# Kernel tuning notes

Measured on AMD Instinct MI355X. Metric: run time of the kernel, lower is better.

Reference implementation:

```python
import jax, jax.numpy as jnp
import numpy as np

B, S, D, H = 8, 1024, 512, 8
DK = D // H
NEG = -1e30  # stands in for -inf; masked probs are zero-filled afterwards, so math matches


def setup_inputs() -> dict:
    rng = jax.random.key(0)
    ks = jax.random.split(rng, 12)
    f = lambda k, shape: jax.random.normal(k, shape, dtype=jnp.float32)
    w = lambda k: f(k, (D, D)) * 0.02  # stored as (in, out); y = x @ W + b
    return {
        "query": f(ks[0], (B, S, D)),
        "key": f(ks[1], (B, S, D)),
        "value": f(ks[2], (B, S, D)),
        "mask": jax.random.randint(ks[3], (B, 1, S), 0, 2, dtype=jnp.int32),
        "Wq": w(ks[4]), "bq": jnp.zeros((D,), jnp.float32),
        "Wk": w(ks[5]), "bk": jnp.zeros((D,), jnp.float32),
        "Wv": w(ks[6]), "bv": jnp.zeros((D,), jnp.float32),
        "Wo": w(ks[7]), "bo": jnp.zeros((D,), jnp.float32),
    }


def reference(query, key, value, mask, Wq, bq, Wk, bk, Wv, bv, Wo, bo):
    # QKV projections -> (B, H, S, DK)
    def proj(x, W, b):
        return (x @ W + b).reshape(B, -1, H, DK).transpose(0, 2, 1, 3)

    q = proj(query, Wq, bq)
    k = proj(key, Wk, bk)
    v = proj(value, Wv, bv)

    scores = jnp.einsum("bhqd,bhkd->bhqk", q, k) / jnp.sqrt(jnp.float32(DK))
    m = (mask[:, None, :, :] == 0)  # (B, 1, 1, S): True where masked out
    scores = jnp.where(m, NEG, scores)
    attn = jax.nn.softmax(scores, axis=-1)
    attn = jnp.where(m, 0.0, attn)  # dropout rate is 0.0 -> identity

    x = jnp.einsum("bhqk,bhkd->bhqd", attn, v)
    x = x.transpose(0, 2, 1, 3).reshape(B, -1, D)  # (B, S, D)
    return x @ Wo + bo
```

## Files before the change

kernel.cpp:

```cpp
#include <hip/hip_runtime.h>
#include <hip/hip_bf16.h>

#define NB 8
#define NS 1024
#define ND 512
#define NH 8
#define NDK 64

typedef __attribute__((ext_vector_type(8))) short bf16x8;
typedef __attribute__((ext_vector_type(4))) short s16x4;
typedef __attribute__((ext_vector_type(4))) float f32x4;
typedef __attribute__((ext_vector_type(16))) float f32x16;

#define QSCALE 0.18033688011112042f
#define NEGBIG -3.0e38f

#define CVTPK(dst, a, b) \
    asm("v_cvt_pk_bf16_f32 %0, %1, %2" : "=v"(dst) : "v"(a), "v"(b))
#define PLSWAP(a, b) \
    asm("v_permlane32_swap_b32 %0, %1" : "+v"(a), "+v"(b))

__device__ __forceinline__ unsigned short bfround(float f) {
    union { float f; unsigned u; } v; v.f = f;
    unsigned u = v.u;
    u += 0x7fffu + ((u >> 16) & 1u);
    return (unsigned short)(u >> 16);
}

__device__ __forceinline__ size_t qf_off(int s, int dk) {
    return ((size_t)(((s >> 5) * 4 + (dk >> 4)) * 64 + ((dk >> 3) & 1) * 32 + (s & 31)) << 3) + (dk & 7);
}
__device__ __forceinline__ size_t kf_off(int s, int dk) {
    return ((size_t)(((s >> 6) * 8 + ((s >> 5) & 1) * 4 + (dk >> 4)) * 64 + ((dk >> 3) & 1) * 32 + (s & 31)) << 3) + (dk & 7);
}
__device__ __forceinline__ size_t vf_off(int s, int dk) {
    return ((size_t)(((s >> 6) * 8 + (dk >> 5) * 4 + ((s >> 4) & 3)) * 64 + ((s >> 3) & 1) * 32 + (dk & 31)) << 3) + (s & 7);
}

__global__ __launch_bounds__(256) void wt_kernel(const float* __restrict__ W0,
                                                 const float* __restrict__ W1,
                                                 const float* __restrict__ W2,
                                                 const float* __restrict__ W3,
                                                 unsigned short* __restrict__ wt) {
    __shared__ float sh[64][65];
    const int z = blockIdx.z;
    const float* W = z == 0 ? W0 : z == 1 ? W1 : z == 2 ? W2 : W3;
    unsigned short* out = wt + (size_t)z * ND * ND;
    const int o0 = blockIdx.x * 64, i0 = blockIdx.y * 64;
    const int tx = threadIdx.x & 63;
    const int ty = threadIdx.x >> 6;
    #pragma unroll
    for (int rr = 0; rr < 16; ++rr) {
        const int row = ty * 16 + rr;
        sh[row][tx] = W[(size_t)(i0 + row) * ND + o0 + tx];
    }
    __syncthreads();
    #pragma unroll
    for (int rr = 0; rr < 16; ++rr) {
        const int row = ty * 16 + rr;
        out[(size_t)(o0 + row) * ND + i0 + tx] = bfround(sh[tx][row]);
    }
}

template <bool A_F32, bool OUT_F32>
__global__ __launch_bounds__(256) void gemm_kernel(
    const void* __restrict__ A0, const void* __restrict__ A1, const void* __restrict__ A2,
    const unsigned short* __restrict__ wt_base, int wt_stride,
    const float* __restrict__ b0, const float* __restrict__ b1, const float* __restrict__ b2,
    void* __restrict__ out_base, size_t out_stride_bytes) {
    __shared__ unsigned short As[128][40];
    __shared__ unsigned short Bs[128][40];
    const int t = threadIdx.x;
    const int lane = t & 63, w = t >> 6;
    const int wr = w >> 1, wc = w & 1;
    const int lr = lane & 15, lg = lane >> 4;
    const int bid = blockIdx.x;
    const int u = (bid & 7) * (gridDim.x >> 3) + (bid >> 3);
    const int xt = u & 3, yt = (u >> 2) & 63, z = u >> 8;
    const void* Ap = z == 0 ? A0 : z == 1 ? A1 : A2;
    const float* bias = z == 0 ? b0 : z == 1 ? b1 : b2;
    const unsigned short* Wt = wt_base + (size_t)z * wt_stride;
    void* outp = (void*)((char*)out_base + (size_t)z * out_stride_bytes);
    const int m0 = yt * 128, n0 = xt * 128;

    f32x4 acc[4][4];
    #pragma unroll
    for (int i = 0; i < 4; ++i)
        #pragma unroll
        for (int j = 0; j < 4; ++j) acc[i][j] = (f32x4){0.f, 0.f, 0.f, 0.f};

    for (int kt = 0; kt < 16; ++kt) {
        const int k0 = kt * 32;
        __syncthreads();
        if (A_F32) {
            const float* A = (const float*)Ap;
            const int mrow = t >> 3, k4 = (t & 7) * 4;
            #pragma unroll
            for (int r = 0; r < 4; ++r) {
                const int m = mrow + 32 * r;
                float4 v = *(const float4*)(A + (size_t)(m0 + m) * ND + k0 + k4);
                unsigned p0, p1;
                CVTPK(p0, v.x, v.y);
                CVTPK(p1, v.z, v.w);
                uint2 pv; pv.x = p0; pv.y = p1;
                *(uint2*)(&As[m][k4]) = pv;
            }
        } else {
            const unsigned short* A = (const unsigned short*)Ap;
            #pragma unroll
            for (int r = 0; r < 2; ++r) {
                const int idx = t + 256 * r;
                const int m = idx >> 2, k8 = (idx & 3) * 8;
                *(bf16x8*)(&As[m][k8]) =
                    *(const bf16x8*)(A + (size_t)(m0 + m) * ND + k0 + k8);
            }
        }
        #pragma unroll
        for (int r = 0; r < 2; ++r) {
            const int idx = t + 256 * r;
            const int n = idx >> 2, k8 = (idx & 3) * 8;
            *(bf16x8*)(&Bs[n][k8]) =
                *(const bf16x8*)(Wt + (size_t)(n0 + n) * ND + k0 + k8);
        }
        __syncthreads();
        bf16x8 af[4], bfv[4];
        #pragma unroll
        for (int mi = 0; mi < 4; ++mi)
            af[mi] = *(const bf16x8*)(&As[wr * 64 + mi * 16 + lr][lg * 8]);
        #pragma unroll
        for (int nj = 0; nj < 4; ++nj)
            bfv[nj] = *(const bf16x8*)(&Bs[wc * 64 + nj * 16 + lr][lg * 8]);
        #pragma unroll
        for (int mi = 0; mi < 4; ++mi)
            #pragma unroll
            for (int nj = 0; nj < 4; ++nj)
                acc[mi][nj] = __builtin_amdgcn_mfma_f32_16x16x32_bf16(
                    af[mi], bfv[nj], acc[mi][nj], 0, 0, 0);
    }

    const float osc = (!OUT_F32 && z == 0) ? QSCALE : 1.0f;
    #pragma unroll
    for (int mi = 0; mi < 4; ++mi) {
        #pragma unroll
        for (int nj = 0; nj < 4; ++nj) {
            const int n = n0 + wc * 64 + nj * 16 + lr;
            const float bv = bias[n];
            #pragma unroll
            for (int r = 0; r < 4; ++r) {
                const int m = m0 + wr * 64 + mi * 16 + lg * 4 + r;
                const float val = (acc[mi][nj][r] + bv) * osc;
                if (OUT_F32) {
                    ((float*)outp)[(size_t)m * ND + n] = val;
                } else {
                    const int bb = m >> 10, s = m & 1023;
                    const int hh = n >> 6, dk = n & 63;
                    const size_t off = z == 0 ? qf_off(s, dk)
                                     : z == 1 ? kf_off(s, dk)
                                              : vf_off(s, dk);
                    ((unsigned short*)outp)[((size_t)(bb * NH + hh) << 16) + off] =
                        bfround(val);
                }
            }
        }
    }
}

struct AttnState {
    f32x16 acc0, acc1;
    float m_st, l_st;
};

__device__ __forceinline__ void attn_step(const bf16x8 (&kf)[8], const bf16x8 (&vv)[8],
                                          const bf16x8 (&qf)[4], int mval,
                                          float* __restrict__ brow, int lane, int hi,
                                          AttnState& st) {
    brow[lane] = mval ? 0.f : NEGBIG;

    f32x16 sc0 = {}, sc1 = {};
    __builtin_amdgcn_s_setprio(1);
    sc0 = __builtin_amdgcn_mfma_f32_32x32x16_bf16(kf[0], qf[0], sc0, 0, 0, 0);
    sc1 = __builtin_amdgcn_mfma_f32_32x32x16_bf16(kf[4], qf[0], sc1, 0, 0, 0);
    sc0 = __builtin_amdgcn_mfma_f32_32x32x16_bf16(kf[1], qf[1], sc0, 0, 0, 0);
    sc1 = __builtin_amdgcn_mfma_f32_32x32x16_bf16(kf[5], qf[1], sc1, 0, 0, 0);
    sc0 = __builtin_amdgcn_mfma_f32_32x32x16_bf16(kf[2], qf[2], sc0, 0, 0, 0);
    sc1 = __builtin_amdgcn_mfma_f32_32x32x16_bf16(kf[6], qf[2], sc1, 0, 0, 0);
    sc0 = __builtin_amdgcn_mfma_f32_32x32x16_bf16(kf[3], qf[3], sc0, 0, 0, 0);
    sc1 = __builtin_amdgcn_mfma_f32_32x32x16_bf16(kf[7], qf[3], sc1, 0, 0, 0);
    __builtin_amdgcn_s_setprio(0);

    {
        const float* bl = brow + 4 * hi;
        #pragma unroll
        for (int mm = 0; mm < 4; ++mm) {
            const f32x4 bv0 = *(const f32x4*)(bl + 8 * mm);
            const f32x4 bv1 = *(const f32x4*)(bl + 32 + 8 * mm);
            #pragma unroll
            for (int c = 0; c < 4; ++c) {
                sc0[4 * mm + c] += bv0[c];
                sc1[4 * mm + c] += bv1[c];
            }
        }
    }

    float tv[16];
    #pragma unroll
    for (int r = 0; r < 16; ++r) tv[r] = fmaxf(sc0[r], sc1[r]);
    #pragma unroll
    for (int s = 8; s > 0; s >>= 1)
        #pragma unroll
        for (int r = 0; r < 16; ++r)
            if (r < s) tv[r] = fmaxf(tv[r], tv[r + s]);
    const float mx = fmaxf(tv[0], __shfl_xor(tv[0], 32));
    const float mn = fmaxf(st.m_st, mx);

    #pragma unroll
    for (int r = 0; r < 16; ++r) {
        sc0[r] = __builtin_amdgcn_exp2f(sc0[r] - mn);
        sc1[r] = __builtin_amdgcn_exp2f(sc1[r] - mn);
    }
    #pragma unroll
    for (int r = 0; r < 16; ++r) tv[r] = sc0[r] + sc1[r];
    #pragma unroll
    for (int s = 8; s > 0; s >>= 1)
        #pragma unroll
        for (int r = 0; r < 16; ++r)
            if (r < s) tv[r] += tv[r + s];
    const float rs = tv[0] + __shfl_xor(tv[0], 32);

    const bool ch = mn > st.m_st;
    if (__any(ch)) {
        const float f = __builtin_amdgcn_exp2f(st.m_st - mn);
        st.l_st = st.l_st * f + rs;
        st.m_st = mn;
        #pragma unroll
        for (int r = 0; r < 16; ++r) { st.acc0[r] *= f; st.acc1[r] *= f; }
    } else {
        st.l_st += rs;
    }

    union U8 { unsigned u[4]; bf16x8 v; };
    bf16x8 pA0, pA1, pB0, pB1;
    {
        unsigned w00, w01, w10, w11, w20, w21, w30, w31;
        CVTPK(w00, sc0[0], sc0[1]);  CVTPK(w01, sc0[2], sc0[3]);
        CVTPK(w10, sc0[4], sc0[5]);  CVTPK(w11, sc0[6], sc0[7]);
        CVTPK(w20, sc0[8], sc0[9]);  CVTPK(w21, sc0[10], sc0[11]);
        CVTPK(w30, sc0[12], sc0[13]); CVTPK(w31, sc0[14], sc0[15]);
        PLSWAP(w00, w10); PLSWAP(w01, w11);
        PLSWAP(w20, w30); PLSWAP(w21, w31);
        U8 f0; f0.u[0] = w00; f0.u[1] = w01; f0.u[2] = w10; f0.u[3] = w11;
        U8 f1; f1.u[0] = w20; f1.u[1] = w21; f1.u[2] = w30; f1.u[3] = w31;
        pA0 = f0.v; pA1 = f1.v;
    }
    {
        unsigned w00, w01, w10, w11, w20, w21, w30, w31;
        CVTPK(w00, sc1[0], sc1[1]);  CVTPK(w01, sc1[2], sc1[3]);
        CVTPK(w10, sc1[4], sc1[5]);  CVTPK(w11, sc1[6], sc1[7]);
        CVTPK(w20, sc1[8], sc1[9]);  CVTPK(w21, sc1[10], sc1[11]);
        CVTPK(w30, sc1[12], sc1[13]); CVTPK(w31, sc1[14], sc1[15]);
        PLSWAP(w00, w10); PLSWAP(w01, w11);
        PLSWAP(w20, w30); PLSWAP(w21, w31);
        U8 f0; f0.u[0] = w00; f0.u[1] = w01; f0.u[2] = w10; f0.u[3] = w11;
        U8 f1; f1.u[0] = w20; f1.u[1] = w21; f1.u[2] = w30; f1.u[3] = w31;
        pB0 = f0.v; pB1 = f1.v;
    }

    __builtin_amdgcn_s_setprio(1);
    st.acc0 = __builtin_amdgcn_mfma_f32_32x32x16_bf16(vv[0], pA0, st.acc0, 0, 0, 0);
    st.acc1 = __builtin_amdgcn_mfma_f32_32x32x16_bf16(vv[4], pA0, st.acc1, 0, 0, 0);
    st.acc0 = __builtin_amdgcn_mfma_f32_32x32x16_bf16(vv[1], pA1, st.acc0, 0, 0, 0);
    st.acc1 = __builtin_amdgcn_mfma_f32_32x32x16_bf16(vv[5], pA1, st.acc1, 0, 0, 0);
    st.acc0 = __builtin_amdgcn_mfma_f32_32x32x16_bf16(vv[2], pB0, st.acc0, 0, 0, 0);
    st.acc1 = __builtin_amdgcn_mfma_f32_32x32x16_bf16(vv[6], pB0, st.acc1, 0, 0, 0);
    st.acc0 = __builtin_amdgcn_mfma_f32_32x32x16_bf16(vv[3], pB1, st.acc0, 0, 0, 0);
    st.acc1 = __builtin_amdgcn_mfma_f32_32x32x16_bf16(vv[7], pB1, st.acc1, 0, 0, 0);
    __builtin_amdgcn_s_setprio(0);
}

__global__ __launch_bounds__(256, 2) void attn_kernel(const unsigned short* __restrict__ QF,
                                                      const unsigned short* __restrict__ KF,
                                                      const unsigned short* __restrict__ VF,
                                                      const int* __restrict__ mask,
                                                      unsigned short* __restrict__ Xb) {
    __shared__ float bias_lds[4][64];
    const int t = threadIdx.x;
    const int lane = t & 63, w = t >> 6;
    const int q32 = lane & 31, hi = lane >> 5;
    const int bid = blockIdx.x;
    const int u = (bid & 7) * 64 + (bid >> 3);
    const int bh = u >> 3, xq = u & 7;
    const int b = bh >> 3, h = bh & 7;
    const int q = xq * 128 + w * 32 + q32;
    const unsigned short* QFh = QF + ((size_t)bh << 16);
    const unsigned short* KFh = KF + ((size_t)bh << 16);
    const unsigned short* VFh = VF + ((size_t)bh << 16);
    const int* mk = mask + b * NS;
    float* brow = &bias_lds[w][0];

    bf16x8 qf[4];
    {
        const unsigned short* Qp = QFh + (size_t)(xq * 16 + w * 4) * 512 + lane * 8;
        qf[0] = *(const bf16x8*)(Qp + 0 * 512);
        qf[1] = *(const bf16x8*)(Qp + 1 * 512);
        qf[2] = *(const bf16x8*)(Qp + 2 * 512);
        qf[3] = *(const bf16x8*)(Qp + 3 * 512);
    }

    AttnState st;
    st.acc0 = (f32x16){}; st.acc1 = (f32x16){};
    st.m_st = -1.0e30f; st.l_st = 0.f;

    bf16x8 kA[8], kB[8], vv[8];

#define LOADK(dst, itx) do {                                                   \
        const unsigned short* _p = KFh + (size_t)(itx) * 4096 + lane * 8;      \
        dst[0] = *(const bf16x8*)(_p + 0 * 512);                               \
        dst[1] = *(const bf16x8*)(_p + 1 * 512);                               \
        dst[2] = *(const bf16x8*)(_p + 2 * 512);                               \
        dst[3] = *(const bf16x8*)(_p + 3 * 512);                               \
        dst[4] = *(const bf16x8*)(_p + 4 * 512);                               \
        dst[5] = *(const bf16x8*)(_p + 5 * 512);                               \
        dst[6] = *(const bf16x8*)(_p + 6 * 512);                               \
        dst[7] = *(const bf16x8*)(_p + 7 * 512);                               \
    } while (0)

#define LOADV(dst, itx) do {                                                   \
        const unsigned short* _p = VFh + (size_t)(itx) * 4096 + lane * 8;      \
        dst[0] = *(const bf16x8*)(_p + 0 * 512);                               \
        dst[1] = *(const bf16x8*)(_p + 1 * 512);                               \
        dst[2] = *(const bf16x8*)(_p + 2 * 512);                               \
        dst[3] = *(const bf16x8*)(_p + 3 * 512);                               \
        dst[4] = *(const bf16x8*)(_p + 4 * 512);                               \
        dst[5] = *(const bf16x8*)(_p + 5 * 512);                               \
        dst[6] = *(const bf16x8*)(_p + 6 * 512);                               \
        dst[7] = *(const bf16x8*)(_p + 7 * 512);                               \
    } while (0)

    LOADK(kA, 0);
    #pragma unroll 1
    for (int ii = 0; ii < 8; ++ii) {
        const int itE = ii * 2, itO = itE + 1;
        const int mE = mk[itE * 64 + lane];
        LOADV(vv, itE);
        LOADK(kB, itO);
        __builtin_amdgcn_sched_barrier(0);
        attn_step(kA, vv, qf, mE, brow, lane, hi, st);
        const int mO = mk[itO * 64 + lane];
        const int itN = itO + 1 > 15 ? 15 : itO + 1;
        LOADV(vv, itO);
        LOADK(kA, itN);
        __builtin_amdgcn_sched_barrier(0);
        attn_step(kB, vv, qf, mO, brow, lane, hi, st);
    }
#undef LOADK
#undef LOADV

    const float inv = st.l_st > 0.f ? 1.f / st.l_st : 0.f;
    unsigned short* Xp = Xb + (size_t)(b * NS + q) * ND + h * 64 + 4 * hi;
    #pragma unroll
    for (int mm = 0; mm < 4; ++mm) {
        unsigned w0, w1;
        CVTPK(w0, st.acc0[4 * mm] * inv, st.acc0[4 * mm + 1] * inv);
        CVTPK(w1, st.acc0[4 * mm + 2] * inv, st.acc0[4 * mm + 3] * inv);
        uint2 pv; pv.x = w0; pv.y = w1;
        *(uint2*)(Xp + 8 * mm) = pv;
        CVTPK(w0, st.acc1[4 * mm] * inv, st.acc1[4 * mm + 1] * inv);
        CVTPK(w1, st.acc1[4 * mm + 2] * inv, st.acc1[4 * mm + 3] * inv);
        pv.x = w0; pv.y = w1;
        *(uint2*)(Xp + 32 + 8 * mm) = pv;
    }
}

extern "C" void kernel_launch(void* const* d_in, const int* in_sizes, int n_in,
                              void* d_out, int out_size, void* d_ws, size_t ws_size,
                              hipStream_t stream) {
    const float* query = (const float*)d_in[0];
    const float* key   = (const float*)d_in[1];
    const float* value = (const float*)d_in[2];
    const int*   mask  = (const int*)d_in[3];
    const float* Wq = (const float*)d_in[4];
    const float* bq = (const float*)d_in[5];
    const float* Wk = (const float*)d_in[6];
    const float* bk = (const float*)d_in[7];
    const float* Wv = (const float*)d_in[8];
    const float* bv = (const float*)d_in[9];
    const float* Wo = (const float*)d_in[10];
    const float* bo = (const float*)d_in[11];

    const size_t HEADSZ = (size_t)NB * NH * NS * NDK;
    unsigned short* wt = (unsigned short*)d_ws;
    unsigned short* QFb = wt + (size_t)4 * ND * ND;
    unsigned short* KFb = QFb + HEADSZ;
    unsigned short* VFb = KFb + HEADSZ;
    unsigned short* Xb  = VFb + HEADSZ;

    wt_kernel<<<dim3(8, 8, 4), 256, 0, stream>>>(Wq, Wk, Wv, Wo, wt);

    gemm_kernel<true, false><<<768, 256, 0, stream>>>(
        query, key, value, wt, ND * ND, bq, bk, bv, (void*)QFb, HEADSZ * 2);

    attn_kernel<<<512, 256, 0, stream>>>(QFb, KFb, VFb, mask, Xb);

    gemm_kernel<false, true><<<256, 256, 0, stream>>>(
        Xb, Xb, Xb, wt + (size_t)3 * ND * ND, 0, bo, bo, bo, d_out, 0);
}
```

Measured before the change: 85.04 us.

## Use direct global-to-LDS loads in GEMMs and split output GEMM into smaller tiles

Splits the templated GEMM into a QKV kernel and an output-projection kernel. Both now fill shared memory with global_load_lds, which writes directly into LDS and skips the register round-trip. The QKV kernel stages fp32 activations in LDS with an XOR swizzle and converts them to bf16 at fragment-read time. The output GEMM moves to 128x64 tiles with 512 blocks to improve CU occupancy. The cost is doubled LDS traffic for the fp32 A tile, unpadded bf16 LDS rows that may bank-conflict, and no overlap between loads and MFMA.

```diff
diff --git a/kernel.cpp b/kernel.cpp
--- a/kernel.cpp
+++ b/kernel.cpp
@@ -8,7 +8,6 @@
 #define NDK 64
 
 typedef __attribute__((ext_vector_type(8))) short bf16x8;
-typedef __attribute__((ext_vector_type(4))) short s16x4;
 typedef __attribute__((ext_vector_type(4))) float f32x4;
 typedef __attribute__((ext_vector_type(16))) float f32x16;
 
@@ -19,6 +18,10 @@
     asm("v_cvt_pk_bf16_f32 %0, %1, %2" : "=v"(dst) : "v"(a), "v"(b))
 #define PLSWAP(a, b) \
     asm("v_permlane32_swap_b32 %0, %1" : "+v"(a), "+v"(b))
+#define GLOAD16(gp, lp)                                                        \
+    __builtin_amdgcn_global_load_lds(                                          \
+        (const __attribute__((address_space(1))) unsigned*)(gp),               \
+        (__attribute__((address_space(3))) unsigned*)(lp), 16, 0, 0)
 
 __device__ __forceinline__ unsigned short bfround(float f) {
     union { float f; unsigned u; } v; v.f = f;
@@ -62,26 +65,30 @@
     }
 }
 
-template <bool A_F32, bool OUT_F32>
-__global__ __launch_bounds__(256) void gemm_kernel(
-    const void* __restrict__ A0, const void* __restrict__ A1, const void* __restrict__ A2,
-    const unsigned short* __restrict__ wt_base, int wt_stride,
+__global__ __launch_bounds__(256) void gemm_qkv(
+    const float* __restrict__ A0, const float* __restrict__ A1, const float* __restrict__ A2,
+    const unsigned short* __restrict__ wt,
     const float* __restrict__ b0, const float* __restrict__ b1, const float* __restrict__ b2,
-    void* __restrict__ out_base, size_t out_stride_bytes) {
-    __shared__ unsigned short As[128][40];
-    __shared__ unsigned short Bs[128][40];
+    unsigned short* __restrict__ outb) {
+    __shared__ float Asf[128 * 32];
+    __shared__ unsigned short Bs[128 * 32];
     const int t = threadIdx.x;
     const int lane = t & 63, w = t >> 6;
     const int wr = w >> 1, wc = w & 1;
     const int lr = lane & 15, lg = lane >> 4;
     const int bid = blockIdx.x;
-    const int u = (bid & 7) * (gridDim.x >> 3) + (bid >> 3);
+    const int u = (bid & 7) * 96 + (bid >> 3);
     const int xt = u & 3, yt = (u >> 2) & 63, z = u >> 8;
-    const void* Ap = z == 0 ? A0 : z == 1 ? A1 : A2;
+    const float* A = z == 0 ? A0 : z == 1 ? A1 : A2;
     const float* bias = z == 0 ? b0 : z == 1 ? b1 : b2;
-    const unsigned short* Wt = wt_base + (size_t)z * wt_stride;
-    void* outp = (void*)((char*)out_base + (size_t)z * out_stride_bytes);
+    const unsigned short* Wt = wt + (size_t)z * ND * ND;
+    unsigned short* outp = outb + (size_t)z * NB * NH * NS * NDK;
     const int m0 = yt * 128, n0 = xt * 128;
+
+    const int a_row = w * 32 + (lane >> 3);
+    const int a_gc = ((lane & 7) ^ (lane >> 3)) << 2;
+    const int b_row = w * 32 + (lane >> 2);
+    const int b_gc = (lane & 3) * 8;
 
     f32x4 acc[4][4];
     #pragma unroll
@@ -92,53 +99,42 @@
     for (int kt = 0; kt < 16; ++kt) {
         const int k0 = kt * 32;
         __syncthreads();
-        if (A_F32) {
-            const float* A = (const float*)Ap;
-            const int mrow = t >> 3, k4 = (t & 7) * 4;
-            #pragma unroll
-            for (int r = 0; r < 4; ++r) {
-                const int m = mrow + 32 * r;
-                float4 v = *(const float4*)(A + (size_t)(m0 + m) * ND + k0 + k4);
-                unsigned p0, p1;
-                CVTPK(p0, v.x, v.y);
-                CVTPK(p1, v.z, v.w);
-                uint2 pv; pv.x = p0; pv.y = p1;
-                *(uint2*)(&As[m][k4]) = pv;
-            }
-        } else {
-            const unsigned short* A = (const unsigned short*)Ap;
-            #pragma unroll
-            for (int r = 0; r < 2; ++r) {
-                const int idx = t + 256 * r;
-                const int m = idx >> 2, k8 = (idx & 3) * 8;
-                *(bf16x8*)(&As[m][k8]) =
-                    *(const bf16x8*)(A + (size_t)(m0 + m) * ND + k0 + k8);
-            }
+        #pragma unroll
+        for (int j = 0; j < 4; ++j)
+            GLOAD16(A + (size_t)(m0 + a_row + j * 8) * ND + k0 + a_gc,
+                    Asf + (w * 4 + j) * 256);
+        #pragma unroll
+        for (int j = 0; j < 2; ++j)
+            GLOAD16(Wt + (size_t)(n0 + b_row + j * 16) * ND + k0 + b_gc,
+                    Bs + (w * 2 + j) * 512);
+        __syncthreads();
+
+        bf16x8 af[4], bfr[4];
+        #pragma unroll
+        for (int mi = 0; mi < 4; ++mi) {
+            const int r = wr * 64 + mi * 16 + lr;
+            const int u0 = (2 * lg) ^ (lr & 7), u1 = (2 * lg + 1) ^ (lr & 7);
+            const f32x4 x0 = *(const f32x4*)(Asf + r * 32 + u0 * 4);
+            const f32x4 x1 = *(const f32x4*)(Asf + r * 32 + u1 * 4);
+            unsigned p0, p1, p2, p3;
+            CVTPK(p0, x0[0], x0[1]); CVTPK(p1, x0[2], x0[3]);
+            CVTPK(p2, x1[0], x1[1]); CVTPK(p3, x1[2], x1[3]);
+            union { unsigned uu[4]; bf16x8 v; } c;
+            c.uu[0] = p0; c.uu[1] = p1; c.uu[2] = p2; c.uu[3] = p3;
+            af[mi] = c.v;
         }
         #pragma unroll
-        for (int r = 0; r < 2; ++r) {
-            const int idx = t + 256 * r;
-            const int n = idx >> 2, k8 = (idx & 3) * 8;
-            *(bf16x8*)(&Bs[n][k8]) =
-                *(const bf16x8*)(Wt + (size_t)(n0 + n) * ND + k0 + k8);
-        }
-        __syncthreads();
-        bf16x8 af[4], bfv[4];
-        #pragma unroll
-        for (int mi = 0; mi < 4; ++mi)
-            af[mi] = *(const bf16x8*)(&As[wr * 64 + mi * 16 + lr][lg * 8]);
-        #pragma unroll
         for (int nj = 0; nj < 4; ++nj)
-            bfv[nj] = *(const bf16x8*)(&Bs[wc * 64 + nj * 16 + lr][lg * 8]);
+            bfr[nj] = *(const bf16x8*)(Bs + (wc * 64 + nj * 16 + lr) * 32 + lg * 8);
         #pragma unroll
         for (int mi = 0; mi < 4; ++mi)
             #pragma unroll
             for (int nj = 0; nj < 4; ++nj)
                 acc[mi][nj] = __builtin_amdgcn_mfma_f32_16x16x32_bf16(
-                    af[mi], bfv[nj], acc[mi][nj], 0, 0, 0);
-    }
-
-    const float osc = (!OUT_F32 && z == 0) ? QSCALE : 1.0f;
+                    af[mi], bfr[nj], acc[mi][nj], 0, 0, 0);
+    }
+
+    const float osc = z == 0 ? QSCALE : 1.0f;
     #pragma unroll
     for (int mi = 0; mi < 4; ++mi) {
         #pragma unroll
@@ -149,17 +145,76 @@
             for (int r = 0; r < 4; ++r) {
                 const int m = m0 + wr * 64 + mi * 16 + lg * 4 + r;
                 const float val = (acc[mi][nj][r] + bv) * osc;
-                if (OUT_F32) {
-                    ((float*)outp)[(size_t)m * ND + n] = val;
-                } else {
-                    const int bb = m >> 10, s = m & 1023;
-                    const int hh = n >> 6, dk = n & 63;
-                    const size_t off = z == 0 ? qf_off(s, dk)
-                                     : z == 1 ? kf_off(s, dk)
-                                              : vf_off(s, dk);
-                    ((unsigned short*)outp)[((size_t)(bb * NH + hh) << 16) + off] =
-                        bfround(val);
-                }
+                const int bb = m >> 10, s = m & 1023;
+                const int hh = n >> 6, dk = n & 63;
+                const size_t off = z == 0 ? qf_off(s, dk)
+                                 : z == 1 ? kf_off(s, dk)
+                                          : vf_off(s, dk);
+                outp[((size_t)(bb * NH + hh) << 16) + off] = bfround(val);
+            }
+        }
+    }
+}
+
+__global__ __launch_bounds__(256) void gemm_out(
+    const unsigned short* __restrict__ Xb, const unsigned short* __restrict__ Wt,
+    const float* __restrict__ bo, float* __restrict__ outp) {
+    __shared__ unsigned short As[128 * 32];
+    __shared__ unsigned short Bs[64 * 32];
+    const int t = threadIdx.x;
+    const int lane = t & 63, w = t >> 6;
+    const int wr = w >> 1, wc = w & 1;
+    const int lr = lane & 15, lg = lane >> 4;
+    const int bid = blockIdx.x;
+    const int u = (bid & 7) * 64 + (bid >> 3);
+    const int xt = u & 7, yt = u >> 3;
+    const int m0 = yt * 128, n0 = xt * 64;
+
+    const int a_row = w * 32 + (lane >> 2);
+    const int b_row = w * 16 + (lane >> 2);
+    const int gc = (lane & 3) * 8;
+
+    f32x4 acc[4][2];
+    #pragma unroll
+    for (int i = 0; i < 4; ++i)
+        #pragma unroll
+        for (int j = 0; j < 2; ++j) acc[i][j] = (f32x4){0.f, 0.f, 0.f, 0.f};
+
+    for (int kt = 0; kt < 16; ++kt) {
+        const int k0 = kt * 32;
+        __syncthreads();
+        #pragma unroll
+        for (int j = 0; j < 2; ++j)
+            GLOAD16(Xb + (size_t)(m0 + a_row + j * 16) * ND + k0 + gc,
+                    As + (w * 2 + j) * 512);
+        GLOAD16(Wt + (size_t)(n0 + b_row) * ND + k0 + gc, Bs + w * 512);
+        __syncthreads();
+
+        bf16x8 af[4], bfr[2];
+        #pragma unroll
+        for (int mi = 0; mi < 4; ++mi)
+            af[mi] = *(const bf16x8*)(As + (wr * 64 + mi * 16 + lr) * 32 + lg * 8);
+        #pragma unroll
+        for (int nj = 0; nj < 2; ++nj)
+            bfr[nj] = *(const bf16x8*)(Bs + (wc * 32 + nj * 16 + lr) * 32 + lg * 8);
+        #pragma unroll
+        for (int mi = 0; mi < 4; ++mi)
+            #pragma unroll
+            for (int nj = 0; nj < 2; ++nj)
+                acc[mi][nj] = __builtin_amdgcn_mfma_f32_16x16x32_bf16(
+                    af[mi], bfr[nj], acc[mi][nj], 0, 0, 0);
+    }
+
+    #pragma unroll
+    for (int mi = 0; mi < 4; ++mi) {
+        #pragma unroll
+        for (int nj = 0; nj < 2; ++nj) {
+            const int n = n0 + wc * 32 + nj * 16 + lr;
+            const float bv = bo[n];
+            #pragma unroll
+            for (int r = 0; r < 4; ++r) {
+                const int m = m0 + wr * 64 + mi * 16 + lg * 4 + r;
+                outp[(size_t)m * ND + n] = acc[mi][nj][r] + bv;
             }
         }
     }
@@ -396,11 +451,9 @@
 
     wt_kernel<<<dim3(8, 8, 4), 256, 0, stream>>>(Wq, Wk, Wv, Wo, wt);
 
-    gemm_kernel<true, false><<<768, 256, 0, stream>>>(
-        query, key, value, wt, ND * ND, bq, bk, bv, (void*)QFb, HEADSZ * 2);
+    gemm_qkv<<<768, 256, 0, stream>>>(query, key, value, wt, bq, bk, bv, QFb);
 
     attn_kernel<<<512, 256, 0, stream>>>(QFb, KFb, VFb, mask, Xb);
 
-    gemm_kernel<false, true><<<256, 256, 0, stream>>>(
-        Xb, Xb, Xb, wt + (size_t)3 * ND * ND, 0, bo, bo, bo, d_out, 0);
-}
+    gemm_out<<<512, 256, 0, stream>>>(Xb, wt + (size_t)3 * ND * ND, bo, (float*)d_out);
+}
```

Measured after the change: 82.56 us. 2.9% less time.
